# Performance work log

Measured on AMD Instinct MI355X. Metric: run time of the kernel, lower is better.

Reference implementation:

```python
import jax, jax.numpy as jnp
import numpy as np

# dims: M=MC samples, B=graphs, K=latent, H=decoder hidden, N=max nodes, P=permutations
M, B, K, H, N, F_DIM, P = 4, 256, 64, 1024, 50, 3, 64
E = N * (N - 1) // 2  # reduced adjacency = strictly lower triangle
COEFF_A = 1.0
BETA = 1.0
TRIL_I, TRIL_J = np.tril_indices(N, -1)


def setup_inputs() -> dict:
    key = jax.random.key(0)
    ks = jax.random.split(key, 12)
    mean = 0.5 * jax.random.normal(ks[0], (B, K), dtype=jnp.float32)
    logvar = 0.1 * jax.random.normal(ks[1], (B, K), dtype=jnp.float32)
    eps = jax.random.normal(ks[2], (M, B, K), dtype=jnp.float32)
    W1 = jax.random.normal(ks[3], (K, H), dtype=jnp.float32) / np.sqrt(K)
    b1 = jnp.zeros((H,), jnp.float32)
    WA = jax.random.normal(ks[4], (H, E), dtype=jnp.float32) / np.sqrt(H)
    bA = jnp.zeros((E,), jnp.float32)
    WF = jax.random.normal(ks[5], (H, N * F_DIM), dtype=jnp.float32) / np.sqrt(H)
    bF = jnp.zeros((N * F_DIM,), jnp.float32)
    # symmetric binary adjacency with zero diagonal
    U = jax.random.bernoulli(ks[6], 0.15, (B, N, N)).astype(jnp.float32)
    Au = jnp.triu(U, 1)
    A_in = Au + jnp.swapaxes(Au, -1, -2)
    # two bernoulli attributes + one one-hot-categorical attribute (over nodes)
    fb = jax.random.bernoulli(ks[7], 0.3, (B, N, 2)).astype(jnp.float32)
    idx = jax.random.randint(ks[8], (B,), 0, N)
    oh = jax.nn.one_hot(idx, N, dtype=jnp.float32)  # (B, N)
    Fx = jnp.concatenate([fb, oh[..., None]], axis=-1)  # (B, N, 3)
    coeff_Fx = jnp.ones((F_DIM,), jnp.float32)
    permutations = jax.vmap(lambda k: jax.random.permutation(k, N))(
        jax.random.split(ks[9], P)).astype(jnp.int32)  # (P, N)
    return dict(mean=mean, logvar=logvar, eps=eps, W1=W1, b1=b1, WA=WA, bA=bA,
                WF=WF, bF=bF, A_in=A_in, Fx=Fx, coeff_Fx=coeff_Fx,
                permutations=permutations)


def _bernoulli_logprob(x, logits):
    # sum of elementwise Bernoulli log-prob over last axis
    return jnp.sum(x * jax.nn.log_sigmoid(logits)
                   + (1.0 - x) * jax.nn.log_sigmoid(-logits), axis=-1)


def reference(mean, logvar, eps, W1, b1, WA, bA, WF, bF, A_in, Fx, coeff_Fx,
              permutations):
    # pathwise (reparametrised) latent samples: (M, B, K)
    Z = mean + jnp.exp(0.5 * logvar) * eps
    # MLP decoder
    h = jax.nn.relu(Z @ W1 + b1)                       # (M, B, H)
    logits_A = h @ WA + bA                              # (M, B, E)
    logits_Fx = (h @ WF + bF).reshape(M, B, N, F_DIM)   # (M, B, N, F)
    # permutation-matched adjacency: A_perm[b,p,i,j] = A_in[b, perm[p,i], perm[p,j]]
    A_perm = A_in[:, permutations[:, :, None], permutations[:, None, :]]  # (B,P,N,N)
    A_red = A_perm[..., TRIL_I, TRIL_J].reshape(B * P, E)                 # (B*P, E)
    lA = jnp.repeat(logits_A, P, axis=1)                                  # (M, B*P, E)
    nce_A = _bernoulli_logprob(A_red, lA).mean(axis=0)                    # (B*P,)
    nce_A = nce_A.reshape(B, P).max(axis=1)                               # (B,)
    # attribute log-probs: two bernoulli (sum over nodes), one categorical over nodes
    lp_bern = jnp.sum(
        Fx[..., :2] * jax.nn.log_sigmoid(logits_Fx[..., :2])
        + (1.0 - Fx[..., :2]) * jax.nn.log_sigmoid(-logits_Fx[..., :2]),
        axis=-2)                                                          # (M, B, 2)
    lp_cat = jnp.sum(Fx[..., 2] * jax.nn.log_softmax(logits_Fx[..., 2], axis=-1),
                     axis=-1)                                             # (M, B)
    nce_Fx = jnp.concatenate([lp_bern.mean(0), lp_cat.mean(0)[:, None]], axis=-1)  # (B, F)
    # KL(q(z|x) || N(0, I))
    kld = 0.5 * jnp.sum(jnp.exp(logvar) + mean ** 2 - 1.0 - logvar, axis=-1)  # (B,)
    return COEFF_A * nce_A + nce_Fx @ coeff_Fx - BETA * kld
```

## Files before the change

### kernel.cpp

```cpp
#include <hip/hip_runtime.h>
#include <math.h>

#define MM 4
#define BB 256
#define KK 64
#define HH 1024
#define NN 50
#define EE 1225
#define PP 64
#define CTOT 1375
#define NPAD 1408


typedef short short8 __attribute__((ext_vector_type(8)));
typedef float floatx4 __attribute__((ext_vector_type(4)));
typedef unsigned short ushort;

__device__ __forceinline__ ushort f2bf(float f) {
    union { float f; unsigned u; } v; v.f = f;
    unsigned r = v.u + 0x7fffu + ((v.u >> 16) & 1u);
    return (ushort)(r >> 16);
}

__device__ __forceinline__ float logsigm(float l) {
    return -(fmaxf(l, 0.0f) + log1pf(expf(-fabsf(l))));
}

__device__ __forceinline__ float wsum64(float v) {
    #pragma unroll
    for (int m = 1; m < 64; m <<= 1) v += __shfl_xor(v, m);
    return v;
}
__device__ __forceinline__ float wmax64(float v) {
    #pragma unroll
    for (int m = 1; m < 64; m <<= 1) v = fmaxf(v, __shfl_xor(v, m));
    return v;
}

__global__ __launch_bounds__(256) void kA(const float* __restrict__ mean,
                                          const float* __restrict__ logvar,
                                          const float* __restrict__ eps,
                                          const float* __restrict__ W1,
                                          const float* __restrict__ b1,
                                          const float* __restrict__ WA,
                                          const float* __restrict__ WF,
                                          const float* __restrict__ A,
                                          const int*   __restrict__ perms,
                                          ushort* __restrict__ hB,
                                          ushort* __restrict__ Wt,
                                          int*   __restrict__ edgesG,
                                          int*   __restrict__ cntG,
                                          float* __restrict__ kldG,
                                          int*   __restrict__ ipG) {
    const int t = threadIdx.x;
    __shared__ float smem[64 * 65];
    __shared__ int cnt;

    if (blockIdx.x < 512) {
        const int b = blockIdx.x >> 1;
        const int half = blockIdx.x & 1;
        float4* z4 = (float4*)smem;
        if (t == 0) cnt = 0;
        if (t < 64) {
            float mv = mean[b * 64 + t];
            float lv = logvar[b * 64 + t];
            float sd = expf(0.5f * lv);
            float4 z;
            z.x = mv + sd * eps[(0 * BB + b) * 64 + t];
            z.y = mv + sd * eps[(1 * BB + b) * 64 + t];
            z.z = mv + sd * eps[(2 * BB + b) * 64 + t];
            z.w = mv + sd * eps[(3 * BB + b) * 64 + t];
            z4[t] = z;
            if (half == 0) {
                float term = 0.5f * (expf(lv) + mv * mv - 1.0f - lv);
                term = wsum64(term);
                if (t == 0) kldG[b] = term;
            }
        }
        __syncthreads();
        const int j0 = half * 512 + t * 2;
        float acc[4][2] = {};
        #pragma unroll 8
        for (int k = 0; k < 64; k++) {
            float2 w = *(const float2*)&W1[k * HH + j0];
            float4 z = z4[k];
            acc[0][0] += z.x * w.x; acc[0][1] += z.x * w.y;
            acc[1][0] += z.y * w.x; acc[1][1] += z.y * w.y;
            acc[2][0] += z.z * w.x; acc[2][1] += z.z * w.y;
            acc[3][0] += z.w * w.x; acc[3][1] += z.w * w.y;
        }
        float2 bb = *(const float2*)&b1[j0];
        #pragma unroll
        for (int m = 0; m < 4; m++) {
            unsigned u0 = ((unsigned)f2bf(fmaxf(acc[m][0] + bb.x, 0.f))) |
                          ((unsigned)f2bf(fmaxf(acc[m][1] + bb.y, 0.f)) << 16);
            *(unsigned*)&hB[(b * 4 + m) * HH + j0] = u0;
        }
        if (half == 0) {
            for (int x = t; x < 2500; x += 256) {
                int i = x / NN, j = x - i * NN;
                if (j < i) {
                    float a = A[b * 2500 + x];
                    if (a != 0.0f) { int id = atomicAdd(&cnt, 1); edgesG[b * 256 + id] = (i << 8) | j; }
                }
            }
            __syncthreads();
            if (t == 0) cntG[b] = cnt;
        }
    } else if (blockIdx.x < 864) {
        const int id = blockIdx.x - 512;
        const int kt = id & 15, nt = id >> 4;
        float* T = smem;
        const int k0 = kt * 64, n0 = nt * 64;
        #pragma unroll
        for (int i = 0; i < 16; i++) {
            int x = i * 256 + t;
            int kk = x >> 6, nn = x & 63;
            int gn = n0 + nn, gk = k0 + kk;
            float v = 0.f;
            if (gn < EE)        v = WA[gk * EE + gn];
            else if (gn < CTOT) v = WF[gk * 150 + (gn - EE)];
            T[kk * 65 + nn] = v;
        }
        __syncthreads();
        #pragma unroll
        for (int i = 0; i < 16; i++) {
            int x = i * 256 + t;
            int nn = x >> 6, kk = x & 63;
            Wt[(n0 + nn) * 1024 + k0 + kk] = f2bf(T[kk * 65 + nn]);
        }
    } else {
        const int id = blockIdx.x - 864;
        for (int x = id * 800 + t; x < (id + 1) * 800; x += 256) {
            int p = x / NN, i = x - p * NN;
            ipG[p * 51 + perms[x]] = i;
        }
    }
}

__global__ __launch_bounds__(256) void k2(const ushort* __restrict__ hB,
                                          const ushort* __restrict__ Wt,
                                          const float* __restrict__ bA,
                                          const float* __restrict__ bF,
                                          float* __restrict__ Lbar,
                                          float* __restrict__ SnegP,
                                          float* __restrict__ lgF) {
    const int ct = blockIdx.x;
    const int rt = blockIdx.y;
    const int t = threadIdx.x;
    const int w = t >> 6, lane = t & 63;
    const int wm = w >> 1, wn = w & 1;
    const int quad = lane >> 4, l16 = lane & 15;
    __shared__ short As[2][32][72];
    __shared__ short Bs[2][64][72];
    floatx4 acc[2] = {};
    const int row0 = rt * 32, col0 = ct * 64;

    const int r0 = t >> 3, koA = (t & 7) * 8;
    const ushort* pA0 = hB + (row0 + r0) * 1024 + koA;
    const ushort* pB0 = Wt + (col0 + r0) * 1024 + koA;
    const ushort* pB1 = pB0 + 32 * 1024;

    short8 ra0, rb0, rb1;
    short8 sa0, sb0, sb1;

#define MFMA_FROM(B) { \
        _Pragma("unroll") \
        for (int kk = 0; kk < 2; kk++) { \
            int ko = kk * 32 + quad * 8; \
            short8 a0 = *(const short8*)&As[B][wm * 16 + l16][ko]; \
            short8 b0 = *(const short8*)&Bs[B][wn * 32 + l16][ko]; \
            short8 b1 = *(const short8*)&Bs[B][wn * 32 + 16 + l16][ko]; \
            acc[0] = __builtin_amdgcn_mfma_f32_16x16x32_bf16(a0, b0, acc[0], 0, 0, 0); \
            acc[1] = __builtin_amdgcn_mfma_f32_16x16x32_bf16(a0, b1, acc[1], 0, 0, 0); \
        } }

    ra0 = *(const short8*)(pA0);
    rb0 = *(const short8*)(pB0);
    rb1 = *(const short8*)(pB1);
    *(short8*)&As[0][r0][koA] = ra0;
    *(short8*)&Bs[0][r0][koA] = rb0;
    *(short8*)&Bs[0][r0 + 32][koA] = rb1;
    ra0 = *(const short8*)(pA0 + 64);
    rb0 = *(const short8*)(pB0 + 64);
    rb1 = *(const short8*)(pB1 + 64);
    __syncthreads();

    #pragma unroll
    for (int ch = 0; ch < 16; ch += 2) {
        if (ch + 2 < 16) {
            const int off = (ch + 2) * 64;
            sa0 = *(const short8*)(pA0 + off);
            sb0 = *(const short8*)(pB0 + off);
            sb1 = *(const short8*)(pB1 + off);
        }
        MFMA_FROM(0)
        *(short8*)&As[1][r0][koA] = ra0;
        *(short8*)&Bs[1][r0][koA] = rb0;
        *(short8*)&Bs[1][r0 + 32][koA] = rb1;
        __syncthreads();
        if (ch + 3 < 16) {
            const int off = (ch + 3) * 64;
            ra0 = *(const short8*)(pA0 + off);
            rb0 = *(const short8*)(pB0 + off);
            rb1 = *(const short8*)(pB1 + off);
        }
        MFMA_FROM(1)
        if (ch + 2 < 16) {
            *(short8*)&As[0][r0][koA] = sa0;
            *(short8*)&Bs[0][r0][koA] = sb0;
            *(short8*)&Bs[0][r0 + 32][koA] = sb1;
            __syncthreads();
        }
    }
#undef MFMA_FROM

    {
        const int grow = row0 + wm * 16 + quad * 4;
        const int b = grow >> 2;
        float sn0 = 0.f, sn1 = 0.f, sn2 = 0.f, sn3 = 0.f;
        #pragma unroll
        for (int ni = 0; ni < 2; ni++) {
            int gc = col0 + wn * 32 + ni * 16 + l16;
            floatx4 a = acc[ni];
            if (gc < EE) {
                float bias = bA[gc];
                float l0 = a[0] + bias, l1 = a[1] + bias, l2 = a[2] + bias, l3 = a[3] + bias;
                Lbar[b * EE + gc] = 0.25f * (l0 + l1 + l2 + l3);
                sn0 += logsigm(l0); sn1 += logsigm(l1); sn2 += logsigm(l2); sn3 += logsigm(l3);
            } else if (gc < CTOT) {
                int c2 = gc - EE;
                float bias = bF[c2];
                lgF[(b * 4 + 0) * 150 + c2] = a[0] + bias;
                lgF[(b * 4 + 1) * 150 + c2] = a[1] + bias;
                lgF[(b * 4 + 2) * 150 + c2] = a[2] + bias;
                lgF[(b * 4 + 3) * 150 + c2] = a[3] + bias;
            }
        }
        #pragma unroll
        for (int msk = 1; msk < 16; msk <<= 1) {
            sn0 += __shfl_xor(sn0, msk);
            sn1 += __shfl_xor(sn1, msk);
            sn2 += __shfl_xor(sn2, msk);
            sn3 += __shfl_xor(sn3, msk);
        }
        if (l16 == 0) {
            const int o = ct * 2 + wn;
            SnegP[(b * 4 + 0) * 44 + o] = sn0;
            SnegP[(b * 4 + 1) * 44 + o] = sn1;
            SnegP[(b * 4 + 2) * 44 + o] = sn2;
            SnegP[(b * 4 + 3) * 44 + o] = sn3;
        }
    }
}

__global__ __launch_bounds__(1024) void k4(const float* __restrict__ Fx,
                                           const float* __restrict__ coeff,
                                           const int* __restrict__ ipG,
                                           const float* __restrict__ Lbar,
                                           const float* __restrict__ SnegP,
                                           const float* __restrict__ lgF,
                                           const int* __restrict__ edgesG,
                                           const int* __restrict__ cntG,
                                           const float* __restrict__ kldG,
                                           float* __restrict__ out) {
    const int b = blockIdx.x;
    const int t = threadIdx.x;
    const int w = t >> 6, lane = t & 63;
    __shared__ int   ip[PP * 51];
    __shared__ float LbF[NN * 51];
    __shared__ int   edges[256];
    __shared__ float lgfs[600];
    __shared__ float mred[4], snegR[4];
    __shared__ float psum[16][64];

    const int ne = cntG[b];
    for (int x = t; x < PP * 51; x += 1024) ip[x] = ipG[x];
    for (int x = t; x < 2500; x += 1024) {
        int i = x / NN, j = x - i * NN;
        if (j < i) {
            float v = Lbar[b * EE + i * (i - 1) / 2 + j];
            LbF[i * 51 + j] = v;
            LbF[j * 51 + i] = v;
        }
    }
    if (t < 600) lgfs[t] = lgF[b * 600 + t];
    if (t < ne) edges[t] = edgesG[b * 256 + t];
    __syncthreads();

    {
        const int ipB = lane * 51;
        float acc = 0.f;
        for (int x = w; x < ne; x += 16) {
            int ed = edges[x];
            int iu = ip[ipB + (ed >> 8)];
            int iv = ip[ipB + (ed & 255)];
            acc += LbF[iu * 51 + iv];
        }
        psum[w][lane] = acc;
    }

    if (w < 4) {
        float l0 = 0.f, l1 = 0.f, l2 = -INFINITY, x0 = 0.f, x1 = 0.f, x2 = 0.f;
        bool v = lane < NN;
        if (v) {
            l0 = lgfs[w * 150 + lane * 3 + 0];
            l1 = lgfs[w * 150 + lane * 3 + 1];
            l2 = lgfs[w * 150 + lane * 3 + 2];
            x0 = Fx[b * 150 + lane * 3 + 0];
            x1 = Fx[b * 150 + lane * 3 + 1];
            x2 = Fx[b * 150 + lane * 3 + 2];
        }
        float mx = wmax64(l2);
        float es = v ? expf(l2 - mx) : 0.f;
        es = wsum64(es);
        float lse = mx + logf(es);
        float val = 0.f;
        if (v) {
            val = coeff[0] * (logsigm(l0) + x0 * l0)
                + coeff[1] * (logsigm(l1) + x1 * l1)
                + coeff[2] * (x2 * (l2 - lse));
        }
        val = wsum64(val);
        float sv = (lane < 44) ? SnegP[(b * 4 + w) * 44 + lane] : 0.f;
        sv = wsum64(sv);
        if (lane == 0) { mred[w] = val; snegR[w] = sv; }
    }
    __syncthreads();

    if (w == 0) {
        float s = psum[0][lane];
        #pragma unroll
        for (int i = 1; i < 16; i++) s += psum[i][lane];
        float dmax = wmax64(s);
        if (lane == 0) {
            float sbar = 0.25f * (snegR[0] + snegR[1] + snegR[2] + snegR[3]);
            float fxv  = 0.25f * (mred[0] + mred[1] + mred[2] + mred[3]);
            out[b] = (sbar + dmax) + fxv - kldG[b];
        }
    }
}

extern "C" void kernel_launch(void* const* d_in, const int* in_sizes, int n_in,
                              void* d_out, int out_size, void* d_ws, size_t ws_size,
                              hipStream_t stream) {
    const float* mean   = (const float*)d_in[0];
    const float* logvar = (const float*)d_in[1];
    const float* eps    = (const float*)d_in[2];
    const float* W1     = (const float*)d_in[3];
    const float* b1     = (const float*)d_in[4];
    const float* WA     = (const float*)d_in[5];
    const float* bA     = (const float*)d_in[6];
    const float* WF     = (const float*)d_in[7];
    const float* bF     = (const float*)d_in[8];
    const float* A      = (const float*)d_in[9];
    const float* Fx     = (const float*)d_in[10];
    const float* coeff  = (const float*)d_in[11];
    const int*   perms  = (const int*)d_in[12];
    float* out = (float*)d_out;

    ushort* Wt   = (ushort*)d_ws;
    ushort* hB   = Wt + NPAD * 1024;
    float*  Lbar = (float*)(hB + 1024 * 1024);
    float*  SnegP = Lbar + BB * EE;
    float*  lgF  = SnegP + 256 * 4 * 44;
    int*    edgesG = (int*)(lgF + 1024 * 150);
    int*    cntG   = edgesG + 256 * 256;
    float*  kldG   = (float*)(cntG + 256);
    int*    ipG    = (int*)(kldG + 256);

    kA<<<dim3(868), dim3(256), 0, stream>>>(mean, logvar, eps, W1, b1, WA, WF, A, perms,
                                            hB, Wt, edgesG, cntG, kldG, ipG);
    k2<<<dim3(22, 32), dim3(256), 0, stream>>>(hB, Wt, bA, bF, Lbar, SnegP, lgF);
    k4<<<dim3(BB), dim3(1024), 0, stream>>>(Fx, coeff, ipG, Lbar, SnegP, lgF,
                                            edgesG, cntG, kldG, out);
}
```

Before: 116.3 us.

## Tile first-layer GEMM into 64x64 shared-memory blocks, split edge extraction into separate blocks

```diff
diff --git a/kernel.cpp b/kernel.cpp
--- a/kernel.cpp
+++ b/kernel.cpp
@@ -53,60 +53,71 @@
                                           float* __restrict__ kldG,
                                           int*   __restrict__ ipG) {
     const int t = threadIdx.x;
-    __shared__ float smem[64 * 65];
+    __shared__ float smem[64 * 65 + 64 * 64];
     __shared__ int cnt;
 
-    if (blockIdx.x < 512) {
-        const int b = blockIdx.x >> 1;
-        const int half = blockIdx.x & 1;
-        float4* z4 = (float4*)smem;
+    if (blockIdx.x < 256) {
+        const int rb = blockIdx.x >> 4, cb = blockIdx.x & 15;
+        float* Zs = smem;
+        float* Ws = smem + 64 * 65;
+        for (int x = t; x < 4096; x += 256) {
+            int row = x >> 6, k = x & 63;
+            int b = rb * 16 + (row >> 2), m = row & 3;
+            float mv = mean[b * 64 + k];
+            float sd = expf(0.5f * logvar[b * 64 + k]);
+            Zs[row * 65 + k] = mv + sd * eps[(m * BB + b) * 64 + k];
+        }
+        for (int x = t; x < 1024; x += 256) {
+            int k = x >> 4, c4 = (x & 15) * 4;
+            *(float4*)&Ws[k * 64 + c4] = *(const float4*)&W1[k * HH + cb * 64 + c4];
+        }
+        __syncthreads();
+        const int tr = t >> 4, tc = t & 15;
+        float acc[4][4] = {};
+        #pragma unroll 8
+        for (int k = 0; k < 64; k++) {
+            float4 w = *(const float4*)&Ws[k * 64 + tc * 4];
+            float z0 = Zs[(tr * 4 + 0) * 65 + k];
+            float z1 = Zs[(tr * 4 + 1) * 65 + k];
+            float z2 = Zs[(tr * 4 + 2) * 65 + k];
+            float z3 = Zs[(tr * 4 + 3) * 65 + k];
+            acc[0][0] += z0 * w.x; acc[0][1] += z0 * w.y; acc[0][2] += z0 * w.z; acc[0][3] += z0 * w.w;
+            acc[1][0] += z1 * w.x; acc[1][1] += z1 * w.y; acc[1][2] += z1 * w.z; acc[1][3] += z1 * w.w;
+            acc[2][0] += z2 * w.x; acc[2][1] += z2 * w.y; acc[2][2] += z2 * w.z; acc[2][3] += z2 * w.w;
+            acc[3][0] += z3 * w.x; acc[3][1] += z3 * w.y; acc[3][2] += z3 * w.z; acc[3][3] += z3 * w.w;
+        }
+        const int j0 = cb * 64 + tc * 4;
+        float4 bb = *(const float4*)&b1[j0];
+        #pragma unroll
+        for (int i = 0; i < 4; i++) {
+            const int grow = rb * 64 + tr * 4 + i;
+            unsigned u0 = ((unsigned)f2bf(fmaxf(acc[i][0] + bb.x, 0.f))) |
+                          ((unsigned)f2bf(fmaxf(acc[i][1] + bb.y, 0.f)) << 16);
+            unsigned u1 = ((unsigned)f2bf(fmaxf(acc[i][2] + bb.z, 0.f))) |
+                          ((unsigned)f2bf(fmaxf(acc[i][3] + bb.w, 0.f)) << 16);
+            uint2 u; u.x = u0; u.y = u1;
+            *(uint2*)&hB[grow * HH + j0] = u;
+        }
+    } else if (blockIdx.x < 512) {
+        const int b = blockIdx.x - 256;
         if (t == 0) cnt = 0;
         if (t < 64) {
             float mv = mean[b * 64 + t];
             float lv = logvar[b * 64 + t];
-            float sd = expf(0.5f * lv);
-            float4 z;
-            z.x = mv + sd * eps[(0 * BB + b) * 64 + t];
-            z.y = mv + sd * eps[(1 * BB + b) * 64 + t];
-            z.z = mv + sd * eps[(2 * BB + b) * 64 + t];
-            z.w = mv + sd * eps[(3 * BB + b) * 64 + t];
-            z4[t] = z;
-            if (half == 0) {
-                float term = 0.5f * (expf(lv) + mv * mv - 1.0f - lv);
-                term = wsum64(term);
-                if (t == 0) kldG[b] = term;
+            float term = 0.5f * (expf(lv) + mv * mv - 1.0f - lv);
+            term = wsum64(term);
+            if (t == 0) kldG[b] = term;
+        }
+        __syncthreads();
+        for (int x = t; x < 2500; x += 256) {
+            int i = x / NN, j = x - i * NN;
+            if (j < i) {
+                float a = A[b * 2500 + x];
+                if (a != 0.0f) { int id = atomicAdd(&cnt, 1); edgesG[b * 256 + id] = (i << 8) | j; }
             }
         }
         __syncthreads();
-        const int j0 = half * 512 + t * 2;
-        float acc[4][2] = {};
-        #pragma unroll 8
-        for (int k = 0; k < 64; k++) {
-            float2 w = *(const float2*)&W1[k * HH + j0];
-            float4 z = z4[k];
-            acc[0][0] += z.x * w.x; acc[0][1] += z.x * w.y;
-            acc[1][0] += z.y * w.x; acc[1][1] += z.y * w.y;
-            acc[2][0] += z.z * w.x; acc[2][1] += z.z * w.y;
-            acc[3][0] += z.w * w.x; acc[3][1] += z.w * w.y;
-        }
-        float2 bb = *(const float2*)&b1[j0];
-        #pragma unroll
-        for (int m = 0; m < 4; m++) {
-            unsigned u0 = ((unsigned)f2bf(fmaxf(acc[m][0] + bb.x, 0.f))) |
-                          ((unsigned)f2bf(fmaxf(acc[m][1] + bb.y, 0.f)) << 16);
-            *(unsigned*)&hB[(b * 4 + m) * HH + j0] = u0;
-        }
-        if (half == 0) {
-            for (int x = t; x < 2500; x += 256) {
-                int i = x / NN, j = x - i * NN;
-                if (j < i) {
-                    float a = A[b * 2500 + x];
-                    if (a != 0.0f) { int id = atomicAdd(&cnt, 1); edgesG[b * 256 + id] = (i << 8) | j; }
-                }
-            }
-            __syncthreads();
-            if (t == 0) cntG[b] = cnt;
-        }
+        if (t == 0) cntG[b] = cnt;
     } else if (blockIdx.x < 864) {
         const int id = blockIdx.x - 512;
         const int kt = id & 15, nt = id >> 4;
```

Result: faster. 112.2 us (-3.6%).
